# Performance work log

Hardware: AMD Instinct MI355X
Metric: run time of the kernel (lower is better)

The kernel has to match this reference:

```python
import jax, jax.numpy as jnp
import numpy as np

B, N, IN_DIM, OUT_DIM, H = 8, 1024, 256, 256, 4
HD = OUT_DIM // H  # head_dim = 64
NEG = -1e9
EPS = 1e-5


def setup_inputs() -> dict:
    key = jax.random.key(0)
    ks = jax.random.split(key, 9)
    h = jax.random.normal(ks[0], (B, N, IN_DIM), dtype=jnp.float32)
    adj = jax.random.randint(ks[1], (N, N), 0, 2, dtype=jnp.int32)
    adj = adj.at[jnp.arange(N), jnp.arange(N)].set(1)  # self loops so no empty rows
    s = 1.0 / np.sqrt(IN_DIM)
    W = jax.random.uniform(ks[2], (H, IN_DIM, HD), jnp.float32, -s, s)
    sa = 1.0 / np.sqrt(2 * HD)
    a1 = jax.random.uniform(ks[3], (H, HD), jnp.float32, -sa, sa)
    a2 = jax.random.uniform(ks[4], (H, HD), jnp.float32, -sa, sa)
    sp = 1.0 / np.sqrt(OUT_DIM)
    proj_w = jax.random.uniform(ks[5], (OUT_DIM, OUT_DIM), jnp.float32, -sp, sp)
    proj_b = jax.random.uniform(ks[6], (OUT_DIM,), jnp.float32, -sp, sp)
    gamma = jnp.ones((OUT_DIM,), jnp.float32)
    beta = jnp.zeros((OUT_DIM,), jnp.float32)
    return {"h": h, "adj": adj, "W": W, "a1": a1, "a2": a2,
            "proj_w": proj_w, "proj_b": proj_b, "gamma": gamma, "beta": beta}


def reference(h, adj, W, a1, a2, proj_w, proj_b, gamma, beta):
    # Wh: [B,H,N,HD]
    Wh = jnp.einsum('bni,hid->bhnd', h, W)
    # Decompose a([Wh_i || Wh_j]) = a1.Wh_i + a2.Wh_j (same math as concat+linear)
    si = jnp.einsum('bhnd,hd->bhn', Wh, a1)  # [B,H,N]
    sj = jnp.einsum('bhnd,hd->bhn', Wh, a2)
    e = jax.nn.leaky_relu(si[:, :, :, None] + sj[:, :, None, :], 0.2)  # [B,H,N,N]
    mask = (adj == 0)  # [N,N]
    e = jnp.where(mask[None, None], NEG, e)
    alpha = jax.nn.softmax(e, axis=-1)
    out = jnp.einsum('bhnm,bhmd->bhnd', alpha, Wh)  # [B,H,N,HD]
    h_multi = out.transpose(0, 2, 1, 3).reshape(B, N, OUT_DIM)  # concat heads
    h_out = jnp.einsum('bnd,od->bno', h_multi, proj_w) + proj_b
    h_out = h_out + h  # residual (in_dim == out_dim)
    mu = jnp.mean(h_out, axis=-1, keepdims=True)
    var = jnp.mean(jnp.square(h_out - mu), axis=-1, keepdims=True)
    return (h_out - mu) * jax.lax.rsqrt(var + EPS) * gamma + beta
```

## Files before the change

kernel.cpp:

```cpp
#include <hip/hip_runtime.h>
#include <hip/hip_bf16.h>

#define NN 1024
#define LOG2E 1.44269504088896f

typedef __attribute__((ext_vector_type(8))) short short8;
typedef __attribute__((ext_vector_type(4))) float floatx4;
typedef __attribute__((ext_vector_type(4))) int intx4;
typedef __attribute__((ext_vector_type(2))) int intx2;

#define WAIT_VM0()   asm volatile("s_waitcnt vmcnt(0)" ::: "memory")
#define WAIT_VM4()   asm volatile("s_waitcnt vmcnt(4)" ::: "memory")
#define WAIT_LGKM0() asm volatile("s_waitcnt lgkmcnt(0)" ::: "memory")
#define SCHED_FENCE() asm volatile("" ::: "memory")

static __device__ __forceinline__ unsigned pk2(float f0, float f1) {
    unsigned u0 = __float_as_uint(f0) + 0x8000u;
    unsigned u1 = __float_as_uint(f1) + 0x8000u;
    return __builtin_amdgcn_perm(u1, u0, 0x07060302u);
}
static __device__ __forceinline__ short8 pk8(floatx4 v0, floatx4 v1) {
    union { intx4 i; short8 s; } u;
    u.i[0] = (int)pk2(v0[0], v0[1]); u.i[1] = (int)pk2(v0[2], v0[3]);
    u.i[2] = (int)pk2(v1[0], v1[1]); u.i[3] = (int)pk2(v1[2], v1[3]);
    return u.s;
}
static __device__ __forceinline__ void load_lds16(const void* gsrc, void* lds) {
    __builtin_amdgcn_global_load_lds(
        (const __attribute__((address_space(1))) void*)gsrc,
        (__attribute__((address_space(3))) void*)lds, 16, 0, 0);
}

__global__ __launch_bounds__(256) void prep_kernel(
    const float* __restrict__ W, const float* __restrict__ proj_w,
    const int* __restrict__ adj,
    __hip_bfloat16* __restrict__ WTb,
    __hip_bfloat16* __restrict__ pwb,
    unsigned* __restrict__ adjm)
{
    int blk = blockIdx.x, t = threadIdx.x;
    if (blk < 16) {
        int o = blk * 16 + (t >> 4);
        int hh = o >> 6, d = o & 63;
        #pragma unroll
        for (int kk = 0; kk < 16; ++kk) {
            int k = (t & 15) + 16 * kk;
            WTb[(size_t)o * 256 + k] = __float2bfloat16(W[((size_t)hh * 256 + k) * 64 + d]);
        }
    } else if (blk < 32) {
        size_t base = (size_t)(blk - 16) * 4096 + (size_t)t * 16;
        #pragma unroll
        for (int k = 0; k < 16; k += 8) {
            floatx4 v0 = *(const floatx4*)(proj_w + base + k);
            floatx4 v1 = *(const floatx4*)(proj_w + base + k + 4);
            *(short8*)(pwb + base + k) = pk8(v0, v1);
        }
    } else {
        int n = (blk - 32) * 8 + (t >> 5);
        int wd = t & 31;
        const int* arow = adj + (size_t)n * NN + wd * 32;
        unsigned bits = 0;
        #pragma unroll
        for (int j4 = 0; j4 < 8; ++j4) {
            intx4 v = *(const intx4*)(arow + j4 * 4);
            #pragma unroll
            for (int j = 0; j < 4; ++j) if (v[j] != 0) bits |= (1u << (j4 * 4 + j));
        }
        adjm[(size_t)n * 32 + wd] = bits;
    }
}

__global__ __launch_bounds__(256) void wh_kernel(
    const float* __restrict__ h,
    const __hip_bfloat16* __restrict__ WTb,
    const float* __restrict__ a1, const float* __restrict__ a2,
    __hip_bfloat16* __restrict__ WhT,
    float* __restrict__ si, float* __restrict__ sj)
{
    int t = threadIdx.x;
    int w = t >> 6, l = t & 63;
    int rl = l & 15, q = l >> 4;
    int r0 = blockIdx.x * 16;
    int bb = r0 >> 10, n0 = r0 & 1023;

    __shared__ __align__(16) __hip_bfloat16 bst[4][4096];
    __shared__ float redsi[4][4][16];
    __shared__ float redsj[4][4][16];

    short8 af[8];
    const float* Arow = h + (size_t)(r0 + rl) * 256 + q * 8;
    #pragma unroll
    for (int k0 = 0; k0 < 8; ++k0) {
        floatx4 v0 = *(const floatx4*)(Arow + k0 * 32);
        floatx4 v1 = *(const floatx4*)(Arow + k0 * 32 + 4);
        af[k0] = pk8(v0, v1);
    }

    #pragma unroll
    for (int k = 0; k < 8; ++k) {
        int row = k * 2 + (l >> 5);
        int g = (l & 31) ^ (row & 7);
        load_lds16(WTb + (size_t)w * 4096 + row * 256 + g * 8, &bst[w][k * 512]);
    }

    #pragma unroll
    for (int j = 0; j < 4; ++j) {
        WAIT_VM0();
        floatx4 acc = {0.f, 0.f, 0.f, 0.f};
        #pragma unroll
        for (int k0 = 0; k0 < 8; ++k0) {
            int p = ((k0 << 2) + q) ^ (rl & 7);
            short8 bf = *(const short8*)(&bst[w][rl * 256 + p * 8]);
            acc = __builtin_amdgcn_mfma_f32_16x16x32_bf16(af[k0], bf, acc, 0, 0, 0);
        }
        WAIT_LGKM0();
        if (j < 3) {
            int ctn = w + 4 * (j + 1);
            #pragma unroll
            for (int k = 0; k < 8; ++k) {
                int row = k * 2 + (l >> 5);
                int g = (l & 31) ^ (row & 7);
                load_lds16(WTb + (size_t)ctn * 4096 + row * 256 + g * 8, &bst[w][k * 512]);
            }
        }

        intx2 pr;
        pr[0] = (int)pk2(acc[0], acc[1]);
        pr[1] = (int)pk2(acc[2], acc[3]);
        *(intx2*)(WhT + ((size_t)(bb * 4 + j) * 64 + w * 16 + rl) * NN + n0 + q * 4) = pr;

        float av1 = a1[j * 64 + w * 16 + rl] * LOG2E;
        float av2 = a2[j * 64 + w * 16 + rl] * LOG2E;
        #pragma unroll
        for (int i = 0; i < 4; ++i) {
            float p1 = acc[i] * av1, p2 = acc[i] * av2;
            #pragma unroll
            for (int off = 1; off < 16; off <<= 1) {
                p1 += __shfl_xor(p1, off, 64);
                p2 += __shfl_xor(p2, off, 64);
            }
            if (rl == 0) { redsi[w][j][q * 4 + i] = p1; redsj[w][j][q * 4 + i] = p2; }
        }
    }
    __syncthreads();

    if (t < 64) {
        int head = t >> 4, row = t & 15;
        si[(size_t)(bb * 4 + head) * NN + n0 + row] =
            redsi[0][head][row] + redsi[1][head][row] + redsi[2][head][row] + redsi[3][head][row];
    } else if (t < 128) {
        int u = t - 64;
        int head = u >> 4, row = u & 15;
        sj[(size_t)(bb * 4 + head) * NN + n0 + row] =
            redsj[0][head][row] + redsj[1][head][row] + redsj[2][head][row] + redsj[3][head][row];
    }
}

__global__ __launch_bounds__(512, 4) void attn_proj_kernel(
    const unsigned* __restrict__ adjm,
    const __hip_bfloat16* __restrict__ WhT,
    const float* __restrict__ si, const float* __restrict__ sj,
    const __hip_bfloat16* __restrict__ pwb,
    const float* __restrict__ h,
    const float* __restrict__ proj_b, const float* __restrict__ gamma,
    const float* __restrict__ beta,
    float* __restrict__ out)
{
    __shared__ __align__(16) char smem[76288];
    auto bst   = reinterpret_cast<__hip_bfloat16 (*)[2][2048]>(smem);
    auto pl    = reinterpret_cast<__hip_bfloat16 (*)[16][40]>(smem + 65536);
    auto hm    = reinterpret_cast<__hip_bfloat16 (*)[264]>(smem + 65536);
    auto red   = reinterpret_cast<float (*)[8][16]>(smem + 65536 + 8448);
    auto lsums = reinterpret_cast<float (*)[4][16]>(smem + 75776);
    float (*accx)[64][20] = reinterpret_cast<float (*)[64][20]>(smem);

    int bx = blockIdx.x, t = threadIdx.x;
    int w = t >> 6, l = t & 63;
    int hh = w & 3, e = w >> 2;
    int rl = l & 15, q = l >> 4;
    int b = bx >> 6, n0 = (bx & 63) * 16;
    int bh = b * 4 + hh;
    int r0 = bx * 16;

    int r = l >> 2, cg = l & 3;
    float sii = si[(size_t)bh * NN + n0 + r];
    const float* sjr = sj + (size_t)bh * NN;
    const unsigned* amrow = adjm + (size_t)(n0 + r) * 32;

    float lsum = 0.f;
    floatx4 acc[4] = { {0,0,0,0}, {0,0,0,0}, {0,0,0,0}, {0,0,0,0} };

    const __hip_bfloat16* Bhead = WhT + (size_t)bh * 64 * NN;

    int srow = l >> 2;
    int sg = (l & 3) ^ (srow & 3);

    #pragma unroll
    for (int k = 0; k < 4; ++k)
        load_lds16(Bhead + (size_t)(k * 16 + srow) * NN + e * 32 + sg * 8, &bst[w][0][k * 512]);

    #pragma unroll 2
    for (int it = 0; it < 16; ++it) {
        int buf = it & 1;
        int mw = it * 64 + e * 32;
        {
            unsigned bits = amrow[it * 2 + e] >> (cg * 8);
            int mb = mw + cg * 8;
            #pragma unroll
            for (int c4 = 0; c4 < 2; ++c4) {
                floatx4 s4 = *(const floatx4*)(sjr + mb + c4 * 4);
                float pv[4];
                #pragma unroll
                for (int k = 0; k < 4; ++k) {
                    float x = sii + s4[k];
                    x = fmaxf(x, 0.2f * x);
                    x = ((bits >> (c4 * 4 + k)) & 1u) ? x : -1e9f;
                    pv[k] = exp2f(x);
                    lsum += pv[k];
                }
                intx2 two;
                two[0] = (int)pk2(pv[0], pv[1]);
                two[1] = (int)pk2(pv[2], pv[3]);
                *(intx2*)(&pl[w][r][cg * 8 + c4 * 4]) = two;
            }
        }
        SCHED_FENCE();
        if (it < 15) {
            int mwn = mw + 64;
            #pragma unroll
            for (int k = 0; k < 4; ++k)
                load_lds16(Bhead + (size_t)(k * 16 + srow) * NN + mwn + sg * 8, &bst[w][buf ^ 1][k * 512]);
            WAIT_VM4();
        } else {
            WAIT_VM0();
        }
        short8 afr = *(const short8*)(&pl[w][rl][q * 8]);
        #pragma unroll
        for (int dt = 0; dt < 4; ++dt) {
            short8 bfr = *(const short8*)(&bst[w][buf][(dt * 16 + rl) * 32 + (q ^ (rl & 3)) * 8]);
            acc[dt] = __builtin_amdgcn_mfma_f32_16x16x32_bf16(afr, bfr, acc[dt], 0, 0, 0);
        }
    }

    lsum += __shfl_xor(lsum, 1, 64);
    lsum += __shfl_xor(lsum, 2, 64);
    if (cg == 0) lsums[e][hh][r] = lsum;

    __syncthreads();

    if (e == 1) {
        #pragma unroll
        for (int dt = 0; dt < 4; ++dt) {
            #pragma unroll
            for (int i = 0; i < 4; ++i)
                accx[hh][l][dt * 4 + i] = acc[dt][i];
        }
    }
    __syncthreads();

    if (e == 0) {
        float riv[4];
        #pragma unroll
        for (int i = 0; i < 4; ++i)
            riv[i] = 1.f / (lsums[0][hh][q * 4 + i] + lsums[1][hh][q * 4 + i]);
        #pragma unroll
        for (int dt = 0; dt < 4; ++dt) {
            #pragma unroll
            for (int i = 0; i < 4; ++i) {
                float v = acc[dt][i] + accx[hh][l][dt * 4 + i];
                unsigned uv = (__float_as_uint(v * riv[i]) + 0x8000u) >> 16;
                hm[q * 4 + i][hh * 64 + dt * 16 + rl] = __ushort_as_bfloat16((unsigned short)uv);
            }
        }
    }
    __syncthreads();

    short8 paf[8];
    #pragma unroll
    for (int k0 = 0; k0 < 8; ++k0) paf[k0] = *(const short8*)(&hm[rl][q * 8 + k0 * 32]);

    floatx4 pacc[2];
    #pragma unroll
    for (int j = 0; j < 2; ++j) {
        int ct = w + 8 * j;
        const __hip_bfloat16* Bp = pwb + (size_t)(ct * 16 + rl) * 256 + q * 8;
        floatx4 a = {0.f, 0.f, 0.f, 0.f};
        #pragma unroll
        for (int k0 = 0; k0 < 8; ++k0) {
            short8 bfp = *(const short8*)(Bp + k0 * 32);
            a = __builtin_amdgcn_mfma_f32_16x16x32_bf16(paf[k0], bfp, a, 0, 0, 0);
        }
        pacc[j] = a;
    }

    float ps[4] = {0.f, 0.f, 0.f, 0.f};
    #pragma unroll
    for (int j = 0; j < 2; ++j) {
        int col = (w + 8 * j) * 16 + rl;
        float pb = proj_b[col];
        #pragma unroll
        for (int i = 0; i < 4; ++i) {
            float v = pacc[j][i] + pb + h[(size_t)(r0 + q * 4 + i) * 256 + col];
            pacc[j][i] = v;
            ps[i] += v;
        }
    }
    #pragma unroll
    for (int i = 0; i < 4; ++i) {
        float s = ps[i];
        #pragma unroll
        for (int off = 1; off < 16; off <<= 1) s += __shfl_xor(s, off, 64);
        ps[i] = s;
    }
    if (rl == 0) {
        for (int i = 0; i < 4; ++i) red[0][w][q * 4 + i] = ps[i];
    }
    __syncthreads();
    float mu[4];
    #pragma unroll
    for (int i = 0; i < 4; ++i) {
        int row = q * 4 + i;
        float s = 0.f;
        #pragma unroll
        for (int ww = 0; ww < 8; ++ww) s += red[0][ww][row];
        mu[i] = s * (1.f / 256.f);
    }
    float vs[4] = {0.f, 0.f, 0.f, 0.f};
    #pragma unroll
    for (int j = 0; j < 2; ++j) {
        #pragma unroll
        for (int i = 0; i < 4; ++i) { float cv = pacc[j][i] - mu[i]; vs[i] += cv * cv; }
    }
    #pragma unroll
    for (int i = 0; i < 4; ++i) {
        float s = vs[i];
        #pragma unroll
        for (int off = 1; off < 16; off <<= 1) s += __shfl_xor(s, off, 64);
        vs[i] = s;
    }
    if (rl == 0) {
        for (int i = 0; i < 4; ++i) red[1][w][q * 4 + i] = vs[i];
    }
    __syncthreads();
    float rs[4];
    #pragma unroll
    for (int i = 0; i < 4; ++i) {
        int row = q * 4 + i;
        float s = 0.f;
        #pragma unroll
        for (int ww = 0; ww < 8; ++ww) s += red[1][ww][row];
        rs[i] = rsqrtf(s * (1.f / 256.f) + 1e-5f);
    }
    #pragma unroll
    for (int j = 0; j < 2; ++j) {
        int col = (w + 8 * j) * 16 + rl;
        float g = gamma[col], be = beta[col];
        #pragma unroll
        for (int i = 0; i < 4; ++i)
            out[(size_t)(r0 + q * 4 + i) * 256 + col] = (pacc[j][i] - mu[i]) * rs[i] * g + be;
    }
}

extern "C" void kernel_launch(void* const* d_in, const int* in_sizes, int n_in,
                              void* d_out, int out_size, void* d_ws, size_t ws_size,
                              hipStream_t stream) {
    const float* h      = (const float*)d_in[0];
    const int*   adj    = (const int*)d_in[1];
    const float* W      = (const float*)d_in[2];
    const float* a1     = (const float*)d_in[3];
    const float* a2     = (const float*)d_in[4];
    const float* proj_w = (const float*)d_in[5];
    const float* proj_b = (const float*)d_in[6];
    const float* gamma  = (const float*)d_in[7];
    const float* beta   = (const float*)d_in[8];
    float* out = (float*)d_out;

    char* ws = (char*)d_ws;
    __hip_bfloat16* WhT = (__hip_bfloat16*)ws;   ws += (size_t)32 * 64 * NN * 2;
    __hip_bfloat16* WTb = (__hip_bfloat16*)ws;   ws += 256 * 256 * 2;
    __hip_bfloat16* pwb = (__hip_bfloat16*)ws;   ws += 256 * 256 * 2;
    float* si = (float*)ws;                      ws += (size_t)32 * NN * 4;
    float* sj = (float*)ws;                      ws += (size_t)32 * NN * 4;
    unsigned* adjm = (unsigned*)ws;              ws += (size_t)NN * 32 * 4;

    prep_kernel<<<160, 256, 0, stream>>>(W, proj_w, adj, WTb, pwb, adjm);
    wh_kernel<<<512, 256, 0, stream>>>(h, WTb, a1, a2, WhT, si, sj);
    attn_proj_kernel<<<512, 512, 0, stream>>>(adjm, WhT, si, sj, pwb, h, proj_b, gamma, beta, out);
}
```

Baseline: 122.6 us.

## Store Wh in pre-swizzled tiled layout for contiguous LDS staging loads

The intermediate Wh tensor is now written by the projection kernel in a tiled layout of 64x32 blocks with the LDS XOR swizzle already applied. The attention kernel can then fetch each tile with fully contiguous per-lane 16-byte loads instead of strided row gathers across the 1024-wide rows. This cuts address arithmetic and improves coalescing of the streamed loads. In exchange the producer's stores become more scattered, and both kernels now depend on a shared, matching layout.

```diff
diff --git a/kernel.cpp b/kernel.cpp
--- a/kernel.cpp
+++ b/kernel.cpp
@@ -74,7 +74,7 @@
     const float* __restrict__ h,
     const __hip_bfloat16* __restrict__ WTb,
     const float* __restrict__ a1, const float* __restrict__ a2,
-    __hip_bfloat16* __restrict__ WhT,
+    __hip_bfloat16* __restrict__ WhTt,
     float* __restrict__ si, float* __restrict__ sj)
 {
     int t = threadIdx.x;
@@ -103,6 +103,13 @@
         load_lds16(WTb + (size_t)w * 4096 + row * 256 + g * 8, &bst[w][k * 512]);
     }
 
+    int d = w * 16 + rl;
+    int s = (n0 & 31) + q * 4;
+    int g = s >> 3;
+    int mi = s & 7;
+    size_t toff = (size_t)d * 32 + ((g ^ (d & 3)) * 8) + mi;
+    size_t tbase = ((size_t)bb * 4) * 32 + (n0 >> 5);
+
     #pragma unroll
     for (int j = 0; j < 4; ++j) {
         WAIT_VM0();
@@ -119,15 +126,15 @@
             #pragma unroll
             for (int k = 0; k < 8; ++k) {
                 int row = k * 2 + (l >> 5);
-                int g = (l & 31) ^ (row & 7);
-                load_lds16(WTb + (size_t)ctn * 4096 + row * 256 + g * 8, &bst[w][k * 512]);
+                int gg = (l & 31) ^ (row & 7);
+                load_lds16(WTb + (size_t)ctn * 4096 + row * 256 + gg * 8, &bst[w][k * 512]);
             }
         }
 
         intx2 pr;
         pr[0] = (int)pk2(acc[0], acc[1]);
         pr[1] = (int)pk2(acc[2], acc[3]);
-        *(intx2*)(WhT + ((size_t)(bb * 4 + j) * 64 + w * 16 + rl) * NN + n0 + q * 4) = pr;
+        *(intx2*)(WhTt + (tbase + (size_t)j * 32) * 2048 + toff) = pr;
 
         float av1 = a1[j * 64 + w * 16 + rl] * LOG2E;
         float av2 = a2[j * 64 + w * 16 + rl] * LOG2E;
@@ -158,7 +165,7 @@
 
 __global__ __launch_bounds__(512, 4) void attn_proj_kernel(
     const unsigned* __restrict__ adjm,
-    const __hip_bfloat16* __restrict__ WhT,
+    const __hip_bfloat16* __restrict__ WhTt,
     const float* __restrict__ si, const float* __restrict__ sj,
     const __hip_bfloat16* __restrict__ pwb,
     const float* __restrict__ h,
@@ -190,14 +197,11 @@
     float lsum = 0.f;
     floatx4 acc[4] = { {0,0,0,0}, {0,0,0,0}, {0,0,0,0}, {0,0,0,0} };
 
-    const __hip_bfloat16* Bhead = WhT + (size_t)bh * 64 * NN;
-
-    int srow = l >> 2;
-    int sg = (l & 3) ^ (srow & 3);
+    const __hip_bfloat16* Tbase = WhTt + ((size_t)bh * 32 + e) * 2048 + l * 8;
 
     #pragma unroll
     for (int k = 0; k < 4; ++k)
-        load_lds16(Bhead + (size_t)(k * 16 + srow) * NN + e * 32 + sg * 8, &bst[w][0][k * 512]);
+        load_lds16(Tbase + k * 512, &bst[w][0][k * 512]);
 
     #pragma unroll 2
     for (int it = 0; it < 16; ++it) {
@@ -226,10 +230,10 @@
         }
         SCHED_FENCE();
         if (it < 15) {
-            int mwn = mw + 64;
+            const __hip_bfloat16* Tn = Tbase + (size_t)(it + 1) * 2 * 2048;
             #pragma unroll
             for (int k = 0; k < 4; ++k)
-                load_lds16(Bhead + (size_t)(k * 16 + srow) * NN + mwn + sg * 8, &bst[w][buf ^ 1][k * 512]);
+                load_lds16(Tn + k * 512, &bst[w][buf ^ 1][k * 512]);
             WAIT_VM4();
         } else {
             WAIT_VM0();
@@ -376,7 +380,7 @@
     float* out = (float*)d_out;
 
     char* ws = (char*)d_ws;
-    __hip_bfloat16* WhT = (__hip_bfloat16*)ws;   ws += (size_t)32 * 64 * NN * 2;
+    __hip_bfloat16* WhTt = (__hip_bfloat16*)ws;  ws += (size_t)32 * 32 * 2048 * 2;
     __hip_bfloat16* WTb = (__hip_bfloat16*)ws;   ws += 256 * 256 * 2;
     __hip_bfloat16* pwb = (__hip_bfloat16*)ws;   ws += 256 * 256 * 2;
     float* si = (float*)ws;                      ws += (size_t)32 * NN * 4;
@@ -384,6 +388,6 @@
     unsigned* adjm = (unsigned*)ws;              ws += (size_t)NN * 32 * 4;
 
     prep_kernel<<<160, 256, 0, stream>>>(W, proj_w, adj, WTb, pwb, adjm);
-    wh_kernel<<<512, 256, 0, stream>>>(h, WTb, a1, a2, WhT, si, sj);
-    attn_proj_kernel<<<512, 512, 0, stream>>>(adjm, WhT, si, sj, pwb, h, proj_b, gamma, beta, out);
-}
+    wh_kernel<<<512, 256, 0, stream>>>(h, WTb, a1, a2, WhTt, si, sj);
+    attn_proj_kernel<<<512, 512, 0, stream>>>(adjm, WhTt, si, sj, pwb, h, proj_b, gamma, beta, out);
+}
```

Result: no change. 121.2 us (-1.2%).
